# Kernel tuning notes

Hardware: AMD Instinct MI355X
Metric: run time of the kernel (lower is better)

## Reference

```python
import jax, jax.numpy as jnp
import numpy as np

HIDDEN = 2048
INPUT = 2048
BATCH = 4096


def setup_inputs() -> dict:
    key = jax.random.key(0)
    ks = jax.random.split(key, 7)
    x = jax.random.normal(ks[0], (BATCH, INPUT), dtype=jnp.float32)
    h = jax.random.normal(ks[1], (BATCH, HIDDEN), dtype=jnp.float32)
    c = jax.random.normal(ks[2], (BATCH, HIDDEN), dtype=jnp.float32)
    # learned parameters (RandomNormal init stddev=0.05 analogue; scale irrelevant for correctness)
    w_ih = jax.random.normal(ks[3], (4, INPUT, HIDDEN), dtype=jnp.float32) * 0.05
    w_hh = jax.random.normal(ks[4], (4, HIDDEN, HIDDEN), dtype=jnp.float32) * 0.05
    b_ih = jax.random.normal(ks[5], (4, HIDDEN), dtype=jnp.float32) * 0.05
    b_hh = jax.random.normal(ks[6], (4, HIDDEN), dtype=jnp.float32) * 0.05
    return {"x": x, "h": h, "c": c, "w_ih": w_ih, "w_hh": w_hh, "b_ih": b_ih, "b_hh": b_hh}


def reference(x, h, c, w_ih, w_hh, b_ih, b_hh):
    # gates: [4, B, H] = x @ w_ih[g] and h @ w_hh[g], batched over gate dim g
    gates = (
        jnp.einsum("bi,gih->gbh", x, w_ih)
        + jnp.einsum("bh,ghk->gbk", h, w_hh)
        + (b_ih + b_hh)[:, None, :]
    )
    ingate = jax.nn.sigmoid(gates[0])
    forgetgate = jax.nn.sigmoid(gates[1])
    cellgate = jnp.tanh(gates[2])
    outgate = jax.nn.sigmoid(gates[3])
    c_new = forgetgate * c + ingate * cellgate
    h_new = outgate * jnp.tanh(c_new)
    return (h_new, c_new)
```

## Files before the change

### kernel.cpp

```cpp
#include <hip/hip_runtime.h>

#define BATCH  4096
#define HIDDEN 2048
#define INPUT  2048
#define KDIM   4096
#define NDIM   8192
#define BM 256
#define BN 256
#define BK 64
#define NT (KDIM / BK)

typedef __attribute__((ext_vector_type(8))) short short8;
typedef __attribute__((ext_vector_type(4))) float float4v;


__device__ __forceinline__ unsigned short f2bf(float f) {
    union { float f; unsigned u; } v; v.f = f;
    unsigned r = v.u + 0x7FFFu + ((v.u >> 16) & 1u);
    return (unsigned short)(r >> 16);
}

__device__ __forceinline__ void gl2lds16(const unsigned short* g, unsigned short* l) {
    __builtin_amdgcn_global_load_lds(
        (const __attribute__((address_space(1))) unsigned int*)g,
        (__attribute__((address_space(3))) unsigned int*)l,
        16, 0, 0);
}

__device__ __forceinline__ float sigm(float x) {
    return 1.0f / (1.0f + __expf(-x));
}
__device__ __forceinline__ float tanh_fast(float x) {
    return 2.0f / (1.0f + __expf(-2.0f * x)) - 1.0f;
}

__device__ __forceinline__ void fence_bar() {
    asm volatile("" ::: "memory");
    __builtin_amdgcn_s_barrier();
    asm volatile("" ::: "memory");
}


__global__ void pack_x_kernel(const float* __restrict__ x, const float* __restrict__ h,
                              unsigned short* __restrict__ Xb) {
    int idx = blockIdx.x * 256 + threadIdx.x;
    int b  = idx >> 9;
    int ko = idx & 511;
    const float* src = (ko < 256) ? (x + (size_t)b * INPUT  + (size_t)ko * 8)
                                  : (h + (size_t)b * HIDDEN + (size_t)(ko - 256) * 8);
    float4 v0 = *(const float4*)(src);
    float4 v1 = *(const float4*)(src + 4);
    union { unsigned short us[8]; uint4 v; } o;
    o.us[0] = f2bf(v0.x); o.us[1] = f2bf(v0.y); o.us[2] = f2bf(v0.z); o.us[3] = f2bf(v0.w);
    o.us[4] = f2bf(v1.x); o.us[5] = f2bf(v1.y); o.us[6] = f2bf(v1.z); o.us[7] = f2bf(v1.w);
    *(uint4*)(Xb + (size_t)b * KDIM + (size_t)ko * 8) = o.v;
}


__global__ void pack_w_kernel(const float* __restrict__ w_ih, const float* __restrict__ w_hh,
                              unsigned short* __restrict__ Wt) {
    __shared__ unsigned short tile[32][136];
    const int k0 = blockIdx.x * 128;
    const int j0 = blockIdx.y * 32;
    const int g  = blockIdx.z;
    const float* src = (k0 < INPUT)
        ? (w_ih + (size_t)g * INPUT  * HIDDEN + (size_t)k0 * HIDDEN + j0)
        : (w_hh + (size_t)g * HIDDEN * HIDDEN + (size_t)(k0 - INPUT) * HIDDEN + j0);

    const int tid = threadIdx.x;
    const int jl  = (tid & 7) * 4;
    const int kl  = (tid >> 3) * 2;
#pragma unroll
    for (int p = 0; p < 2; ++p) {
        const int k = kl + p * 64;
        float4 v0 = *(const float4*)(src + (size_t)k * HIDDEN + jl);
        float4 v1 = *(const float4*)(src + (size_t)(k + 1) * HIDDEN + jl);
        unsigned p0 = (unsigned)f2bf(v0.x) | ((unsigned)f2bf(v1.x) << 16);
        unsigned p1 = (unsigned)f2bf(v0.y) | ((unsigned)f2bf(v1.y) << 16);
        unsigned p2 = (unsigned)f2bf(v0.z) | ((unsigned)f2bf(v1.z) << 16);
        unsigned p3 = (unsigned)f2bf(v0.w) | ((unsigned)f2bf(v1.w) << 16);
        *(unsigned*)&tile[jl + 0][kl + p * 64] = p0;
        *(unsigned*)&tile[jl + 1][kl + p * 64] = p1;
        *(unsigned*)&tile[jl + 2][kl + p * 64] = p2;
        *(unsigned*)&tile[jl + 3][kl + p * 64] = p3;
    }
    __syncthreads();

#pragma unroll
    for (int p = 0; p < 2; ++p) {
        const int cch = tid + p * 256;
        const int j   = cch >> 4;
        const int k8  = cch & 15;
        uint4 v = *(const uint4*)&tile[j][k8 * 8];
        *(uint4*)(Wt + (size_t)(4 * (j0 + j) + g) * KDIM + k0 + k8 * 8) = v;
    }
}


__global__ __launch_bounds__(512, 2)
void gemm_kernel(const unsigned short* __restrict__ A,
                 const unsigned short* __restrict__ B,
                 const float* __restrict__ c,
                 const float* __restrict__ b_ih,
                 const float* __restrict__ b_hh,
                 float* __restrict__ out) {
    extern __shared__ unsigned short lds[];
    unsigned short* cA = lds;
    unsigned short* nA = lds + 16384;
    unsigned short* cB = lds + 32768;
    unsigned short* nB = lds + 49152;

    const int tid  = threadIdx.x;
    const int wid  = tid >> 6;
    const int lane = tid & 63;
    const int ln   = lane & 15;
    const int kq   = lane >> 4;
    const int wmr  = (wid >> 2) * 128;
    const int wnr  = (wid & 3) * 64;
    const int m0   = blockIdx.y * BM;
    const int n0   = blockIdx.x * BN;

    const int srow  = tid >> 3;
    const int scol8 = (tid & 7) ^ (srow & 7);
    const unsigned short* gA[4];
    const unsigned short* gB[4];
#pragma unroll
    for (int cN = 0; cN < 4; ++cN) {
        gA[cN] = A + (size_t)(m0 + cN * 64 + srow) * KDIM + scol8 * 8;
        gB[cN] = B + (size_t)(n0 + cN * 64 + srow) * KDIM + scol8 * 8;
    }
    const int dOff = tid * 8;

    const int abase = (wmr + ln) * 64;
    const int bbase = (wnr + ln) * 64;
    const int sk0 = ((0 + kq) ^ (ln & 7)) * 8;
    const int sk1 = ((4 + kq) ^ (ln & 7)) * 8;

    float4v acc[8][4];
#pragma unroll
    for (int i = 0; i < 8; ++i)
#pragma unroll
        for (int j = 0; j < 4; ++j)
            acc[i][j] = (float4v){0.f, 0.f, 0.f, 0.f};

#define STAGE_A(cN) gl2lds16(gA[cN] + konext, nA + (cN) * 4096 + dOff)
#define STAGE_B(cN) gl2lds16(gB[cN] + konext, nB + (cN) * 4096 + dOff)

    {
#pragma unroll
        for (int cN = 0; cN < 4; ++cN) gl2lds16(gB[cN], cB + cN * 4096 + dOff);
#pragma unroll
        for (int cN = 0; cN < 4; ++cN) gl2lds16(gA[cN], cA + cN * 4096 + dOff);
    }

    short8 bf[4][2];

    for (int T = 0; T < NT; ++T) {
        const bool last = (T == NT - 1);
        const int konext = (T + 1) * BK;

        if (!last) {
            STAGE_B(0); STAGE_B(1); STAGE_B(2); STAGE_B(3);
            STAGE_A(0); STAGE_A(1); STAGE_A(2); STAGE_A(3);
            asm volatile("s_waitcnt vmcnt(8)" ::: "memory");
        } else {
            asm volatile("s_waitcnt vmcnt(0)" ::: "memory");
        }
        fence_bar();
        {
#pragma unroll
            for (int ni = 0; ni < 4; ++ni) {
                bf[ni][0] = *(const short8*)(cB + bbase + ni * 1024 + sk0);
                bf[ni][1] = *(const short8*)(cB + bbase + ni * 1024 + sk1);
            }
            short8 a00 = *(const short8*)(cA + abase + sk0);
            short8 a01 = *(const short8*)(cA + abase + sk1);
            short8 a10 = *(const short8*)(cA + abase + 1024 + sk0);
            short8 a11 = *(const short8*)(cA + abase + 1024 + sk1);
            __builtin_amdgcn_s_setprio(1);
#pragma unroll
            for (int ni = 0; ni < 4; ++ni)
                acc[0][ni] = __builtin_amdgcn_mfma_f32_16x16x32_bf16(a00, bf[ni][0], acc[0][ni], 0, 0, 0);
#pragma unroll
            for (int ni = 0; ni < 4; ++ni)
                acc[1][ni] = __builtin_amdgcn_mfma_f32_16x16x32_bf16(a10, bf[ni][0], acc[1][ni], 0, 0, 0);
#pragma unroll
            for (int ni = 0; ni < 4; ++ni)
                acc[0][ni] = __builtin_amdgcn_mfma_f32_16x16x32_bf16(a01, bf[ni][1], acc[0][ni], 0, 0, 0);
#pragma unroll
            for (int ni = 0; ni < 4; ++ni)
                acc[1][ni] = __builtin_amdgcn_mfma_f32_16x16x32_bf16(a11, bf[ni][1], acc[1][ni], 0, 0, 0);
            __builtin_amdgcn_s_setprio(0);
        }
        fence_bar();

#pragma unroll
        for (int ph = 1; ph < 4; ++ph) {
            short8 a00 = *(const short8*)(cA + abase + (2 * ph) * 1024 + sk0);
            short8 a01 = *(const short8*)(cA + abase + (2 * ph) * 1024 + sk1);
            short8 a10 = *(const short8*)(cA + abase + (2 * ph + 1) * 1024 + sk0);
            short8 a11 = *(const short8*)(cA + abase + (2 * ph + 1) * 1024 + sk1);
            fence_bar();
            __builtin_amdgcn_s_setprio(1);
#pragma unroll
            for (int ni = 0; ni < 4; ++ni)
                acc[2 * ph][ni] = __builtin_amdgcn_mfma_f32_16x16x32_bf16(a00, bf[ni][0], acc[2 * ph][ni], 0, 0, 0);
#pragma unroll
            for (int ni = 0; ni < 4; ++ni)
                acc[2 * ph + 1][ni] = __builtin_amdgcn_mfma_f32_16x16x32_bf16(a10, bf[ni][0], acc[2 * ph + 1][ni], 0, 0, 0);
#pragma unroll
            for (int ni = 0; ni < 4; ++ni)
                acc[2 * ph][ni] = __builtin_amdgcn_mfma_f32_16x16x32_bf16(a01, bf[ni][1], acc[2 * ph][ni], 0, 0, 0);
#pragma unroll
            for (int ni = 0; ni < 4; ++ni)
                acc[2 * ph + 1][ni] = __builtin_amdgcn_mfma_f32_16x16x32_bf16(a11, bf[ni][1], acc[2 * ph + 1][ni], 0, 0, 0);
            __builtin_amdgcn_s_setprio(0);
            fence_bar();
        }

        unsigned short* t0 = cA; cA = nA; nA = t0;
        unsigned short* t1 = cB; cB = nB; nB = t1;
    }
#undef STAGE_A
#undef STAGE_B

    const int qg = lane & 3;
    const int tq = (lane & 15) >> 2;
    const int jb = (n0 >> 2) + (wnr >> 2);
    const size_t HB = (size_t)BATCH * HIDDEN;

    float bia[4][4];
#pragma unroll
    for (int ni = 0; ni < 4; ++ni) {
        const int jgq = jb + ni * 4 + tq;
        bia[ni][0] = b_ih[jgq]              + b_hh[jgq];
        bia[ni][1] = b_ih[HIDDEN + jgq]     + b_hh[HIDDEN + jgq];
        bia[ni][2] = b_ih[2 * HIDDEN + jgq] + b_hh[2 * HIDDEN + jgq];
        bia[ni][3] = b_ih[3 * HIDDEN + jgq] + b_hh[3 * HIDDEN + jgq];
    }

#pragma unroll
    for (int mi = 0; mi < 8; ++mi) {
        float fgv[4], pv[4], ogv[4];
#pragma unroll
        for (int ni = 0; ni < 4; ++ni) {
            float4v v = acc[mi][ni];
            float t1 = __shfl_xor((qg & 1) ? v[0] : v[1], 1);
            float t2 = __shfl_xor((qg & 1) ? v[2] : v[3], 1);
            v[0] = (qg & 1) ? t1 : v[0];
            v[1] = (qg & 1) ? v[1] : t1;
            v[2] = (qg & 1) ? t2 : v[2];
            v[3] = (qg & 1) ? v[3] : t2;
            float t3 = __shfl_xor((qg & 2) ? v[0] : v[2], 2);
            float t4 = __shfl_xor((qg & 2) ? v[1] : v[3], 2);
            v[0] = (qg & 2) ? t3 : v[0];
            v[1] = (qg & 2) ? t4 : v[1];
            v[2] = (qg & 2) ? v[2] : t3;
            v[3] = (qg & 2) ? v[3] : t4;

            const float ig = sigm(v[0] + bia[ni][0]);
            const float fg = sigm(v[1] + bia[ni][1]);
            const float cg = tanh_fast(v[2] + bia[ni][2]);
            const float og = sigm(v[3] + bia[ni][3]);
            fgv[ni] = fg;
            pv[ni]  = ig * cg;
            ogv[ni] = og;
        }
#define TRANS_T(a)                                                        \
        {                                                                 \
            float u1 = __shfl_xor((tq & 1) ? a[0] : a[1], 4);             \
            float u2 = __shfl_xor((tq & 1) ? a[2] : a[3], 4);             \
            a[0] = (tq & 1) ? u1 : a[0];                                  \
            a[1] = (tq & 1) ? a[1] : u1;                                  \
            a[2] = (tq & 1) ? u2 : a[2];                                  \
            a[3] = (tq & 1) ? a[3] : u2;                                  \
            float u3 = __shfl_xor((tq & 2) ? a[0] : a[2], 8);             \
            float u4 = __shfl_xor((tq & 2) ? a[1] : a[3], 8);             \
            a[0] = (tq & 2) ? u3 : a[0];                                  \
            a[2] = (tq & 2) ? a[2] : u3;                                  \
            a[1] = (tq & 2) ? u4 : a[1];                                  \
            a[3] = (tq & 2) ? a[3] : u4;                                  \
        }
        TRANS_T(fgv);
        TRANS_T(pv);
        TRANS_T(ogv);
#undef TRANS_T

        const int row = m0 + wmr + mi * 16 + kq * 4 + qg;
        const int jcol = jb + 4 * tq;
        const float4 cv = *(const float4*)(c + (size_t)row * HIDDEN + jcol);
        float4 hn4, cn4;
        {
            const float cn0 = fgv[0] * cv.x + pv[0];
            const float cn1 = fgv[1] * cv.y + pv[1];
            const float cn2 = fgv[2] * cv.z + pv[2];
            const float cn3 = fgv[3] * cv.w + pv[3];
            cn4.x = cn0; cn4.y = cn1; cn4.z = cn2; cn4.w = cn3;
            hn4.x = ogv[0] * tanh_fast(cn0);
            hn4.y = ogv[1] * tanh_fast(cn1);
            hn4.z = ogv[2] * tanh_fast(cn2);
            hn4.w = ogv[3] * tanh_fast(cn3);
        }
        *(float4*)(out + (size_t)row * HIDDEN + jcol)      = hn4;
        *(float4*)(out + HB + (size_t)row * HIDDEN + jcol) = cn4;
    }
}


extern "C" void kernel_launch(void* const* d_in, const int* in_sizes, int n_in,
                              void* d_out, int out_size, void* d_ws, size_t ws_size,
                              hipStream_t stream) {
    const float* x    = (const float*)d_in[0];
    const float* h    = (const float*)d_in[1];
    const float* c    = (const float*)d_in[2];
    const float* w_ih = (const float*)d_in[3];
    const float* w_hh = (const float*)d_in[4];
    const float* b_ih = (const float*)d_in[5];
    const float* b_hh = (const float*)d_in[6];
    float* out = (float*)d_out;

    const size_t XB_BYTES = (size_t)BATCH * KDIM * 2;
    unsigned short* Xb = (unsigned short*)d_ws;
    unsigned short* Wt = (unsigned short*)((char*)d_ws + XB_BYTES);

    hipLaunchKernelGGL(pack_x_kernel, dim3((size_t)BATCH * KDIM / 8 / 256), dim3(256), 0, stream,
                       x, h, Xb);
    hipLaunchKernelGGL(pack_w_kernel, dim3(KDIM / 128, HIDDEN / 32, 4), dim3(256), 0, stream,
                       w_ih, w_hh, Wt);
    hipLaunchKernelGGL(gemm_kernel, dim3(NDIM / BN, BATCH / BM), dim3(512), 131072, stream,
                       Xb, Wt, c, b_ih, b_hh, out);
}
```

Baseline: 487.4 us.

## Drop intra-tile barriers, remap workgroups for XCD locality, relax launch bounds

Removes the per-phase workgroup barriers inside each K-tile, leaving one barrier before and one after the MFMA phases. Workgroup IDs are remapped so that blocks sent round-robin to the 8 XCDs get contiguous output tiles, which should improve L2 reuse. The minimum-blocks hint in launch bounds drops from 2 to 1, giving the compiler more registers at a possible cost in occupancy. Without the barriers, waves drift further apart, which loses the lockstep ping-pong scheduling but cuts sync stalls.

```diff
diff --git a/kernel.cpp b/kernel.cpp
--- a/kernel.cpp
+++ b/kernel.cpp
@@ -97,7 +97,7 @@
 }
 
 
-__global__ __launch_bounds__(512, 2)
+__global__ __launch_bounds__(512, 1)
 void gemm_kernel(const unsigned short* __restrict__ A,
                  const unsigned short* __restrict__ B,
                  const float* __restrict__ c,
@@ -117,8 +117,13 @@
     const int kq   = lane >> 4;
     const int wmr  = (wid >> 2) * 128;
     const int wnr  = (wid & 3) * 64;
-    const int m0   = blockIdx.y * BM;
-    const int n0   = blockIdx.x * BN;
+
+    const int nwgx = NDIM / BN;
+    const int L    = blockIdx.y * nwgx + blockIdx.x;
+    const int cpx  = (nwgx * (BATCH / BM)) >> 3;
+    const int Ls   = (L & 7) * cpx + (L >> 3);
+    const int m0   = (Ls / nwgx) * BM;
+    const int n0   = (Ls % nwgx) * BN;
 
     const int srow  = tid >> 3;
     const int scol8 = (tid & 7) ^ (srow & 7);
@@ -167,40 +172,18 @@
             asm volatile("s_waitcnt vmcnt(0)" ::: "memory");
         }
         fence_bar();
-        {
-#pragma unroll
-            for (int ni = 0; ni < 4; ++ni) {
-                bf[ni][0] = *(const short8*)(cB + bbase + ni * 1024 + sk0);
-                bf[ni][1] = *(const short8*)(cB + bbase + ni * 1024 + sk1);
-            }
-            short8 a00 = *(const short8*)(cA + abase + sk0);
-            short8 a01 = *(const short8*)(cA + abase + sk1);
-            short8 a10 = *(const short8*)(cA + abase + 1024 + sk0);
-            short8 a11 = *(const short8*)(cA + abase + 1024 + sk1);
-            __builtin_amdgcn_s_setprio(1);
-#pragma unroll
-            for (int ni = 0; ni < 4; ++ni)
-                acc[0][ni] = __builtin_amdgcn_mfma_f32_16x16x32_bf16(a00, bf[ni][0], acc[0][ni], 0, 0, 0);
-#pragma unroll
-            for (int ni = 0; ni < 4; ++ni)
-                acc[1][ni] = __builtin_amdgcn_mfma_f32_16x16x32_bf16(a10, bf[ni][0], acc[1][ni], 0, 0, 0);
-#pragma unroll
-            for (int ni = 0; ni < 4; ++ni)
-                acc[0][ni] = __builtin_amdgcn_mfma_f32_16x16x32_bf16(a01, bf[ni][1], acc[0][ni], 0, 0, 0);
-#pragma unroll
-            for (int ni = 0; ni < 4; ++ni)
-                acc[1][ni] = __builtin_amdgcn_mfma_f32_16x16x32_bf16(a11, bf[ni][1], acc[1][ni], 0, 0, 0);
-            __builtin_amdgcn_s_setprio(0);
-        }
-        fence_bar();
-
-#pragma unroll
-        for (int ph = 1; ph < 4; ++ph) {
+
+#pragma unroll
+        for (int ni = 0; ni < 4; ++ni) {
+            bf[ni][0] = *(const short8*)(cB + bbase + ni * 1024 + sk0);
+            bf[ni][1] = *(const short8*)(cB + bbase + ni * 1024 + sk1);
+        }
+#pragma unroll
+        for (int ph = 0; ph < 4; ++ph) {
             short8 a00 = *(const short8*)(cA + abase + (2 * ph) * 1024 + sk0);
             short8 a01 = *(const short8*)(cA + abase + (2 * ph) * 1024 + sk1);
             short8 a10 = *(const short8*)(cA + abase + (2 * ph + 1) * 1024 + sk0);
             short8 a11 = *(const short8*)(cA + abase + (2 * ph + 1) * 1024 + sk1);
-            fence_bar();
             __builtin_amdgcn_s_setprio(1);
 #pragma unroll
             for (int ni = 0; ni < 4; ++ni)
@@ -215,8 +198,9 @@
             for (int ni = 0; ni < 4; ++ni)
                 acc[2 * ph + 1][ni] = __builtin_amdgcn_mfma_f32_16x16x32_bf16(a11, bf[ni][1], acc[2 * ph + 1][ni], 0, 0, 0);
             __builtin_amdgcn_s_setprio(0);
-            fence_bar();
-        }
+        }
+
+        fence_bar();
 
         unsigned short* t0 = cA; cA = nA; nA = t0;
         unsigned short* t1 = cB; cB = nB; nB = t1;
```

Measured after the change: 488.8 us. About the same (+0.3%).

## Interleave next-tile global-to-LDS staging across four MFMA phases per K tile

Applied to the files above, without the earlier changes.

Instead of issuing all eight next-tile global->LDS loads at the start of each K iteration, the loads are spread across four compute phases, two chunks each. Each phase now covers one K-half for four M rows, and the B fragments for both K-halves are kept in registers. Launch bounds drop from 2 to 1 blocks per SM, so the compiler may use more registers. The aim is to overlap memory traffic with MFMA work more evenly and cut stalls at the start of each iteration, at the cost of lower occupancy and a tighter wait (vmcnt(2)) that depends on load ordering.

```diff
diff --git a/kernel.cpp b/kernel.cpp
--- a/kernel.cpp
+++ b/kernel.cpp
@@ -97,7 +97,7 @@
 }
 
 
-__global__ __launch_bounds__(512, 2)
+__global__ __launch_bounds__(512, 1)
 void gemm_kernel(const unsigned short* __restrict__ A,
                  const unsigned short* __restrict__ B,
                  const float* __restrict__ c,
@@ -153,70 +153,80 @@
         for (int cN = 0; cN < 4; ++cN) gl2lds16(gA[cN], cA + cN * 4096 + dOff);
     }
 
-    short8 bf[4][2];
+    short8 bf0[4], bf1[4];
+    short8 af[4];
 
     for (int T = 0; T < NT; ++T) {
         const bool last = (T == NT - 1);
         const int konext = (T + 1) * BK;
 
-        if (!last) {
-            STAGE_B(0); STAGE_B(1); STAGE_B(2); STAGE_B(3);
-            STAGE_A(0); STAGE_A(1); STAGE_A(2); STAGE_A(3);
-            asm volatile("s_waitcnt vmcnt(8)" ::: "memory");
-        } else {
-            asm volatile("s_waitcnt vmcnt(0)" ::: "memory");
-        }
-        fence_bar();
-        {
-#pragma unroll
-            for (int ni = 0; ni < 4; ++ni) {
-                bf[ni][0] = *(const short8*)(cB + bbase + ni * 1024 + sk0);
-                bf[ni][1] = *(const short8*)(cB + bbase + ni * 1024 + sk1);
-            }
-            short8 a00 = *(const short8*)(cA + abase + sk0);
-            short8 a01 = *(const short8*)(cA + abase + sk1);
-            short8 a10 = *(const short8*)(cA + abase + 1024 + sk0);
-            short8 a11 = *(const short8*)(cA + abase + 1024 + sk1);
-            __builtin_amdgcn_s_setprio(1);
+        if (!last) { STAGE_B(0); STAGE_B(1); }
+        if (!last) asm volatile("s_waitcnt vmcnt(2)" ::: "memory");
+        else       asm volatile("s_waitcnt vmcnt(0)" ::: "memory");
+        fence_bar();
+#pragma unroll
+        for (int ni = 0; ni < 4; ++ni)
+            bf0[ni] = *(const short8*)(cB + bbase + ni * 1024 + sk0);
+#pragma unroll
+        for (int r = 0; r < 4; ++r)
+            af[r] = *(const short8*)(cA + abase + r * 1024 + sk0);
+        __builtin_amdgcn_s_setprio(1);
+#pragma unroll
+        for (int mi = 0; mi < 4; ++mi)
 #pragma unroll
             for (int ni = 0; ni < 4; ++ni)
-                acc[0][ni] = __builtin_amdgcn_mfma_f32_16x16x32_bf16(a00, bf[ni][0], acc[0][ni], 0, 0, 0);
+                acc[mi][ni] = __builtin_amdgcn_mfma_f32_16x16x32_bf16(
+                    af[mi], bf0[ni], acc[mi][ni], 0, 0, 0);
+        __builtin_amdgcn_s_setprio(0);
+        fence_bar();
+
+#pragma unroll
+        for (int ni = 0; ni < 4; ++ni)
+            bf1[ni] = *(const short8*)(cB + bbase + ni * 1024 + sk1);
+#pragma unroll
+        for (int r = 0; r < 4; ++r)
+            af[r] = *(const short8*)(cA + abase + r * 1024 + sk1);
+        if (!last) { STAGE_B(2); STAGE_B(3); }
+        fence_bar();
+        __builtin_amdgcn_s_setprio(1);
+#pragma unroll
+        for (int mi = 0; mi < 4; ++mi)
 #pragma unroll
             for (int ni = 0; ni < 4; ++ni)
-                acc[1][ni] = __builtin_amdgcn_mfma_f32_16x16x32_bf16(a10, bf[ni][0], acc[1][ni], 0, 0, 0);
+                acc[mi][ni] = __builtin_amdgcn_mfma_f32_16x16x32_bf16(
+                    af[mi], bf1[ni], acc[mi][ni], 0, 0, 0);
+        __builtin_amdgcn_s_setprio(0);
+        fence_bar();
+
+#pragma unroll
+        for (int r = 0; r < 4; ++r)
+            af[r] = *(const short8*)(cA + abase + (4 + r) * 1024 + sk0);
+        if (!last) { STAGE_A(0); STAGE_A(1); }
+        fence_bar();
+        __builtin_amdgcn_s_setprio(1);
+#pragma unroll
+        for (int mi = 0; mi < 4; ++mi)
 #pragma unroll
             for (int ni = 0; ni < 4; ++ni)
-                acc[0][ni] = __builtin_amdgcn_mfma_f32_16x16x32_bf16(a01, bf[ni][1], acc[0][ni], 0, 0, 0);
+                acc[4 + mi][ni] = __builtin_amdgcn_mfma_f32_16x16x32_bf16(
+                    af[mi], bf0[ni], acc[4 + mi][ni], 0, 0, 0);
+        __builtin_amdgcn_s_setprio(0);
+        fence_bar();
+
+#pragma unroll
+        for (int r = 0; r < 4; ++r)
+            af[r] = *(const short8*)(cA + abase + (4 + r) * 1024 + sk1);
+        if (!last) { STAGE_A(2); STAGE_A(3); }
+        fence_bar();
+        __builtin_amdgcn_s_setprio(1);
+#pragma unroll
+        for (int mi = 0; mi < 4; ++mi)
 #pragma unroll
             for (int ni = 0; ni < 4; ++ni)
-                acc[1][ni] = __builtin_amdgcn_mfma_f32_16x16x32_bf16(a11, bf[ni][1], acc[1][ni], 0, 0, 0);
-            __builtin_amdgcn_s_setprio(0);
-        }
-        fence_bar();
-
-#pragma unroll
-        for (int ph = 1; ph < 4; ++ph) {
-            short8 a00 = *(const short8*)(cA + abase + (2 * ph) * 1024 + sk0);
-            short8 a01 = *(const short8*)(cA + abase + (2 * ph) * 1024 + sk1);
-            short8 a10 = *(const short8*)(cA + abase + (2 * ph + 1) * 1024 + sk0);
-            short8 a11 = *(const short8*)(cA + abase + (2 * ph + 1) * 1024 + sk1);
-            fence_bar();
-            __builtin_amdgcn_s_setprio(1);
-#pragma unroll
-            for (int ni = 0; ni < 4; ++ni)
-                acc[2 * ph][ni] = __builtin_amdgcn_mfma_f32_16x16x32_bf16(a00, bf[ni][0], acc[2 * ph][ni], 0, 0, 0);
-#pragma unroll
-            for (int ni = 0; ni < 4; ++ni)
-                acc[2 * ph + 1][ni] = __builtin_amdgcn_mfma_f32_16x16x32_bf16(a10, bf[ni][0], acc[2 * ph + 1][ni], 0, 0, 0);
-#pragma unroll
-            for (int ni = 0; ni < 4; ++ni)
-                acc[2 * ph][ni] = __builtin_amdgcn_mfma_f32_16x16x32_bf16(a01, bf[ni][1], acc[2 * ph][ni], 0, 0, 0);
-#pragma unroll
-            for (int ni = 0; ni < 4; ++ni)
-                acc[2 * ph + 1][ni] = __builtin_amdgcn_mfma_f32_16x16x32_bf16(a11, bf[ni][1], acc[2 * ph + 1][ni], 0, 0, 0);
-            __builtin_amdgcn_s_setprio(0);
-            fence_bar();
-        }
+                acc[4 + mi][ni] = __builtin_amdgcn_mfma_f32_16x16x32_bf16(
+                    af[mi], bf1[ni], acc[4 + mi][ni], 0, 0, 0);
+        __builtin_amdgcn_s_setprio(0);
+        fence_bar();
 
         unsigned short* t0 = cA; cA = nA; nA = t0;
         unsigned short* t1 = cB; cB = nB; nB = t1;
```

Result: no change. 495.3 us (+1.6%).
